# Kernel optimization log

Measured on AMD Instinct MI355X. Metric: run time of the kernel, lower is better.

The kernel has to match this reference:

```python
import jax, jax.numpy as jnp
import numpy as np

NX = 48
N_TILES = 6
C_IN = 16
H = 32            # node_hidden_channels
EH = 64           # edge_hidden_channels
N_STEPS = 4       # num_step_message_passing
N_NODES = N_TILES * NX * NX


def _build_edges(nx, n_tiles):
    # 4-neighbor (up/down/left/right, wraparound) connectivity per tile
    ii = np.arange(nx * nx, dtype=np.int32).reshape(nx, nx)
    srcs, dsts = [], []
    for t in range(n_tiles):
        off = t * nx * nx
        for ax, sh in ((0, 1), (0, -1), (1, 1), (1, -1)):
            srcs.append(off + np.roll(ii, sh, axis=ax).ravel())
            dsts.append(off + ii.ravel())
    return np.concatenate(srcs), np.concatenate(dsts)


def setup_inputs() -> dict:
    key = jax.random.key(0)
    ks = jax.random.split(key, 16)
    src_np, dst_np = _build_edges(NX, N_TILES)
    E = src_np.shape[0]  # 55296
    s = 0.1
    return {
        "in_node_feats": jax.random.normal(ks[0], (2, N_TILES, NX, NX, C_IN), jnp.float32),
        "edge_feats": jax.random.normal(ks[1], (E, 2), jnp.float32),
        "src": jnp.asarray(src_np, jnp.int32),
        "dst": jnp.asarray(dst_np, jnp.int32),
        # project_node_feats: Linear(C_IN,H) -> relu -> Linear(H,H)
        "pW1": jax.random.normal(ks[2], (C_IN, H), jnp.float32) * s,
        "pb1": jnp.zeros((H,), jnp.float32),
        "pW2": jax.random.normal(ks[3], (H, H), jnp.float32) * s,
        "pb2": jnp.zeros((H,), jnp.float32),
        # edge network: Linear(2,EH) -> relu -> Linear(EH, H*H)
        "eW1": jax.random.normal(ks[4], (2, EH), jnp.float32) * s,
        "eb1": jnp.zeros((EH,), jnp.float32),
        "eW2": jax.random.normal(ks[5], (EH, H * H), jnp.float32) * (s / 4.0),
        "eb2": jnp.zeros((H * H,), jnp.float32),
        # NNConv bias
        "conv_b": jnp.zeros((H,), jnp.float32),
        # GRU (single layer): gate order r, z, n (PyTorch)
        "gWih": jax.random.normal(ks[6], (3 * H, H), jnp.float32) * s,
        "gWhh": jax.random.normal(ks[7], (3 * H, H), jnp.float32) * s,
        "gbih": jnp.zeros((3 * H,), jnp.float32),
        "gbhh": jnp.zeros((3 * H,), jnp.float32),
    }


def reference(in_node_feats, edge_feats, src, dst,
              pW1, pb1, pW2, pb2, eW1, eb1, eW2, eb2,
              conv_b, gWih, gWhh, gbih, gbhh):
    shp = in_node_feats.shape           # (B, T, nx, ny, Cin)
    B = shp[0]
    N = shp[1] * shp[2] * shp[3]
    x = in_node_feats.reshape(B, N, shp[-1])
    # project node features
    x = jnp.maximum(x @ pW1 + pb1, 0.0) @ pW2 + pb2      # (B, N, H)
    # per-edge weight matrices (shared across batch and steps)
    We = jnp.maximum(edge_feats @ eW1 + eb1, 0.0) @ eW2 + eb2
    We = We.reshape(-1, H, H)                             # (E, H, H)
    h = x
    seg = jax.vmap(lambda m: jax.ops.segment_sum(m, dst, num_segments=N))
    for _ in range(N_STEPS):
        # NNConv: gather src feats, per-edge matmul, scatter-sum to dst, + bias
        msg = jnp.einsum('beh,eho->beo', x[:, src], We)   # (B, E, H)
        x = jnp.maximum(seg(msg) + conv_b, 0.0)           # relu(conv)
        # GRU cell (seq_len = 1)
        gx = x @ gWih.T + gbih
        gh = h @ gWhh.T + gbhh
        xr, xz, xn = jnp.split(gx, 3, axis=-1)
        hr, hz, hn = jnp.split(gh, 3, axis=-1)
        r = jax.nn.sigmoid(xr + hr)
        z = jax.nn.sigmoid(xz + hz)
        n = jnp.tanh(xn + r * hn)
        h = (1.0 - z) * n + z * h
        x = h
    return x.reshape(shp[:4] + (H,))
```

## Files before the change

kernel.cpp:

```cpp
#include <hip/hip_runtime.h>
#include <stdint.h>

constexpr int NB   = 2;
constexpr int NN   = 13824;
constexpr int NE   = 55296;
constexpr int H    = 32;
constexpr int EHID = 64;
constexpr int HH   = 1024;
constexpr int TILE = 2304;
constexpr int NXC  = 48;

typedef float f32x4 __attribute__((ext_vector_type(4)));
typedef short s16x8 __attribute__((ext_vector_type(8)));
typedef unsigned int u32x2 __attribute__((ext_vector_type(2)));
typedef unsigned int u32x4 __attribute__((ext_vector_type(4)));
typedef __attribute__((address_space(1))) unsigned int as1_uint;
typedef __attribute__((address_space(3))) unsigned int as3_uint;

static __device__ __forceinline__ unsigned short f2bf(float f) {
    unsigned u = __float_as_uint(f);
    return (unsigned short)((u + 0x7fffu + ((u >> 16) & 1u)) >> 16);
}
static __device__ __forceinline__ unsigned packbf(float lo, float hi) {
    return (unsigned)f2bf(lo) | ((unsigned)f2bf(hi) << 16);
}
static __device__ __forceinline__ void gload16(const void* g, void* l) {
    __builtin_amdgcn_global_load_lds((const as1_uint*)g, (as3_uint*)l, 16, 0, 0);
}
static __device__ __forceinline__ float sigf(float v) {
    return 1.0f / (1.0f + __expf(-v));
}
static __device__ __forceinline__ float tanhfast(float v) {
    return 1.0f - 2.0f / (1.0f + __expf(2.0f * v));
}

__global__ void __launch_bounds__(256)
k_pre(const float* __restrict__ ef, const float* __restrict__ eW1,
      const float* __restrict__ eb1, unsigned short* __restrict__ aB,
      const float* __restrict__ eW2, const float* __restrict__ eb2,
      unsigned short* __restrict__ BpT, float* __restrict__ eb2p,
      const float* __restrict__ in, const float* __restrict__ pW1,
      const float* __restrict__ pb1, const float* __restrict__ pW2,
      const float* __restrict__ pb2, float* __restrict__ S0,
      unsigned short* __restrict__ xb0,
      const float* __restrict__ gWih, const float* __restrict__ gWhh,
      unsigned short* __restrict__ gWb) {
    int blk = blockIdx.x;
    if (blk < 3456) {
        int t = blk * 256 + threadIdx.x;
        int e = t >> 4, kq = (t & 15) * 4;
        float f0 = ef[e * 2], f1 = ef[e * 2 + 1];
        u32x2 w;
#pragma unroll
        for (int q = 0; q < 2; q++) {
            int k = kq + q * 2;
            float v0 = fmaxf(f0 * eW1[k]     + f1 * eW1[64 + k]     + eb1[k],     0.f);
            float v1 = fmaxf(f0 * eW1[k + 1] + f1 * eW1[64 + k + 1] + eb1[k + 1], 0.f);
            w[q] = packbf(v0, v1);
        }
        *(u32x2*)(aB + e * 64 + kq) = w;
    } else if (blk < 3520) {
        int t = (blk - 3456) * 256 + threadIdx.x;
        int jp = t >> 4, kq = (t & 15) * 4;
        int src_col = (jp & 31) * 32 + (jp >> 5);
        u32x2 w;
#pragma unroll
        for (int q = 0; q < 2; q++) {
            int k = kq + q * 2;
            w[q] = packbf(eW2[k * HH + src_col], eW2[(k + 1) * HH + src_col]);
        }
        *(u32x2*)(BpT + jp * 64 + kq) = w;
        if (kq == 0) eb2p[jp] = eb2[src_col];
    } else if (blk < 6976) {
        int t = (blk - 3520) * 256 + threadIdx.x;
        int p = t >> 5;
        int l = t & 31;
        float iv = (l < 16) ? in[p * 16 + l] : 0.f;
        float hid = pb1[l];
#pragma unroll
        for (int c = 0; c < 16; c++) hid = fmaf(__shfl(iv, c, 32), pW1[c * H + l], hid);
        hid = fmaxf(hid, 0.f);
        float out = pb2[l];
#pragma unroll
        for (int h = 0; h < 32; h++) out = fmaf(__shfl(hid, h, 32), pW2[h * H + l], out);
        S0[p * H + l]  = out;
        xb0[p * H + l] = f2bf(out);
    } else {
        int idx = (blk - 6976) * 256 + threadIdx.x;
        gWb[idx] = f2bf(idx < 3072 ? gWih[idx] : gWhh[idx - 3072]);
    }
}

__global__ void __launch_bounds__(256)
k_gemm(const unsigned short* __restrict__ Bp, const unsigned short* __restrict__ Ae,
       const float* __restrict__ eb2p, unsigned short* __restrict__ C) {
    __shared__ unsigned char lds[32768] __attribute__((aligned(16)));
    const int tid  = threadIdx.x;
    const int wv   = tid >> 6;
    const int lane = tid & 63;
    const int lr   = lane & 15;
    const int lg   = lane >> 4;
    const int jbt  = blockIdx.x;
    const int ebt  = blockIdx.y;

    const unsigned char* Ag = (const unsigned char*)Bp + (size_t)jbt * 16384;
    const unsigned char* Bg = (const unsigned char*)Ae + (size_t)ebt * 16384;

#pragma unroll
    for (int c = 0; c < 4; c++) {
        int fbase = (wv * 4 + c) * 1024;
        int f  = fbase + lane * 16;
        int sw = f ^ (((f >> 7) & 7) << 4);
        gload16(Ag + sw, lds + fbase);
        gload16(Bg + sw, lds + 16384 + fbase);
    }
    asm volatile("s_waitcnt vmcnt(0)" ::: "memory");
    __syncthreads();

    const int wm = wv >> 1, wn = wv & 1;
    f32x4 acc[4][4] = {};
#pragma unroll
    for (int kk = 0; kk < 2; kk++) {
        s16x8 af[4], bf[4];
#pragma unroll
        for (int i = 0; i < 4; i++) {
            int la = ((wm * 64 + i * 16 + lr) * 64 + kk * 32 + lg * 8) * 2;
            la ^= ((la >> 7) & 7) << 4;
            af[i] = *(const s16x8*)(lds + la);
            int lb = ((wn * 64 + i * 16 + lr) * 64 + kk * 32 + lg * 8) * 2;
            lb ^= ((lb >> 7) & 7) << 4;
            bf[i] = *(const s16x8*)(lds + 16384 + lb);
        }
#pragma unroll
        for (int i = 0; i < 4; i++)
#pragma unroll
            for (int j = 0; j < 4; j++)
                acc[i][j] = __builtin_amdgcn_mfma_f32_16x16x32_bf16(af[i], bf[j], acc[i][j], 0, 0, 0);
    }

    float bias[4][4];
#pragma unroll
    for (int i = 0; i < 4; i++)
#pragma unroll
        for (int r = 0; r < 4; r++)
            bias[i][r] = eb2p[jbt * 128 + wm * 64 + i * 16 + lg * 4 + r];

    __syncthreads();
#pragma unroll
    for (int i = 0; i < 4; i++) {
#pragma unroll
        for (int j = 0; j < 4; j++) {
            int el    = wn * 64 + j * 16 + lr;
            int jbase = wm * 64 + i * 16 + lg * 4;
            int L0 = el * 256 + jbase * 2;
            int ph = L0 ^ ((el & 7) << 4);
            u32x2 w;
            w[0] = packbf(acc[i][j][0] + bias[i][0], acc[i][j][1] + bias[i][1]);
            w[1] = packbf(acc[i][j][2] + bias[i][2], acc[i][j][3] + bias[i][3]);
            *(u32x2*)(lds + ph) = w;
        }
    }
    __syncthreads();

    const int q  = (ebt * 128) / TILE;
    const int i0 = (ebt * 128) % TILE;
    const int tt = q >> 2, kk2 = q & 3;
    const size_t nbase = (size_t)tt * TILE + i0;
#pragma unroll
    for (int pass = 0; pass < 8; pass++) {
        int L2 = pass * 4096 + tid * 16;
        int el = L2 >> 8;
        int ph = L2 ^ ((el & 7) << 4);
        u32x4 v = *(const u32x4*)(lds + ph);
        size_t drow = (nbase + el) * 4 + kk2;
        *(u32x4*)((unsigned char*)C + drow * 2048 + (size_t)jbt * 256 + (L2 & 255)) = v;
    }
}

__global__ void __launch_bounds__(256)
k_step3(const unsigned short* __restrict__ xb_in,
        const float* __restrict__ h_in,
        const unsigned short* __restrict__ WeTn,
        const float* __restrict__ conv_b,
        const unsigned short* __restrict__ gWb,
        const float* __restrict__ gbih, const float* __restrict__ gbhh,
        float* __restrict__ h_out, unsigned short* __restrict__ xb_out) {
    __shared__ unsigned short cv[2][8][32];
    const int tid  = threadIdx.x;
    const int wv   = tid >> 6;
    const int l    = tid & 63;
    const int cl   = l & 15;
    const int kg   = l >> 4;
    const int bsel = cl & 1;
    const int n0   = blockIdx.x * 8;

    int srcs[2][4];
#pragma unroll
    for (int un = 0; un < 2; ++un) {
        int n = n0 + wv * 2 + un;
        int t = n / TILE;
        int i = n - t * TILE;
        int r = i / NXC;
        int c = i - r * NXC;
        int bt = t * TILE;
        int rm = (r == 0) ? NXC - 1 : r - 1;
        int rp = (r == NXC - 1) ? 0 : r + 1;
        int cm = (c == 0) ? NXC - 1 : c - 1;
        int cp = (c == NXC - 1) ? 0 : c + 1;
        srcs[un][0] = bt + rm * NXC + c;
        srcs[un][1] = bt + rp * NXC + c;
        srcs[un][2] = bt + r * NXC + cm;
        srcs[un][3] = bt + r * NXC + cp;
    }

    s16x8 af[2][4][2];
#pragma unroll
    for (int un = 0; un < 2; ++un) {
        const unsigned short* wp = WeTn + ((size_t)(n0 + wv * 2 + un) * 4) * HH;
#pragma unroll
        for (int k = 0; k < 4; ++k) {
            af[un][k][0] = *(const s16x8*)(wp + k * HH + cl * 32 + kg * 8);
            af[un][k][1] = *(const s16x8*)(wp + k * HH + 512 + cl * 32 + kg * 8);
        }
    }

    f32x4 a[2][2] = {};
#pragma unroll
    for (int un = 0; un < 2; ++un) {
#pragma unroll
        for (int k = 0; k < 4; ++k) {
            s16x8 bfr = *(const s16x8*)(xb_in + ((size_t)(bsel * NN + srcs[un][k])) * 32 + kg * 8);
            a[un][0] = __builtin_amdgcn_mfma_f32_16x16x32_bf16(af[un][k][0], bfr, a[un][0], 0, 0, 0);
            a[un][1] = __builtin_amdgcn_mfma_f32_16x16x32_bf16(af[un][k][1], bfr, a[un][1], 0, 0, 0);
        }
    }

    f32x4 cb0 = *(const f32x4*)(conv_b + kg * 4);
    f32x4 cb1 = *(const f32x4*)(conv_b + 16 + kg * 4);
    if (cl < 2) {
#pragma unroll
        for (int un = 0; un < 2; ++un) {
            int nl = wv * 2 + un;
            unsigned* cp32 = (unsigned*)&cv[cl][nl][0];
            cp32[kg * 2]     = packbf(fmaxf(a[un][0][0] + cb0[0], 0.f), fmaxf(a[un][0][1] + cb0[1], 0.f));
            cp32[kg * 2 + 1] = packbf(fmaxf(a[un][0][2] + cb0[2], 0.f), fmaxf(a[un][0][3] + cb0[3], 0.f));
            cp32[8 + kg * 2]     = packbf(fmaxf(a[un][1][0] + cb1[0], 0.f), fmaxf(a[un][1][1] + cb1[1], 0.f));
            cp32[8 + kg * 2 + 1] = packbf(fmaxf(a[un][1][2] + cb1[2], 0.f), fmaxf(a[un][1][3] + cb1[3], 0.f));
        }
    }
    __syncthreads();

    if (wv == 0) {
        s16x8 ax = *(const s16x8*)&cv[cl >> 3][cl & 7][kg * 8];
        s16x8 ah = *(const s16x8*)(xb_in + ((size_t)(cl >> 3) * NN + n0 + (cl & 7)) * 32 + kg * 8);

        f32x4 accx[6], acch[6];
#pragma unroll
        for (int jb = 0; jb < 6; ++jb) {
            s16x8 wx = *(const s16x8*)(gWb + (jb * 16 + cl) * 32 + kg * 8);
            s16x8 wh = *(const s16x8*)(gWb + 3072 + (jb * 16 + cl) * 32 + kg * 8);
            f32x4 z0 = {};
            f32x4 z1 = {};
            accx[jb] = __builtin_amdgcn_mfma_f32_16x16x32_bf16(ax, wx, z0, 0, 0, 0);
            acch[jb] = __builtin_amdgcn_mfma_f32_16x16x32_bf16(ah, wh, z1, 0, 0, 0);
        }

        float bihR[2] = {gbih[cl],      gbih[16 + cl]};
        float bihZ[2] = {gbih[32 + cl], gbih[48 + cl]};
        float bihN[2] = {gbih[64 + cl], gbih[80 + cl]};
        float bhhR[2] = {gbhh[cl],      gbhh[16 + cl]};
        float bhhZ[2] = {gbhh[32 + cl], gbhh[48 + cl]};
        float bhhN[2] = {gbhh[64 + cl], gbhh[80 + cl]};

#pragma unroll
        for (int hb = 0; hb < 2; ++hb) {
#pragma unroll
            for (int ri = 0; ri < 4; ++ri) {
                int rrow = kg * 4 + ri;
                size_t m = (size_t)(rrow >> 3) * NN + n0 + (rrow & 7);
                float rg = sigf(accx[hb][ri] + acch[hb][ri] + bihR[hb] + bhhR[hb]);
                float zg = sigf(accx[2 + hb][ri] + acch[2 + hb][ri] + bihZ[hb] + bhhZ[hb]);
                float ng = tanhfast((accx[4 + hb][ri] + bihN[hb]) +
                                    rg * (acch[4 + hb][ri] + bhhN[hb]));
                float ho = h_in[m * 32 + hb * 16 + cl];
                float hn = fmaf(zg, ho - ng, ng);
                h_out[m * 32 + hb * 16 + cl]  = hn;
                xb_out[m * 32 + hb * 16 + cl] = f2bf(hn);
            }
        }
    }
}

extern "C" void kernel_launch(void* const* d_in, const int* in_sizes, int n_in,
                              void* d_out, int out_size, void* d_ws, size_t ws_size,
                              hipStream_t stream) {
    const float* in_nodes = (const float*)d_in[0];
    const float* ef       = (const float*)d_in[1];
    const float* pW1      = (const float*)d_in[4];
    const float* pb1      = (const float*)d_in[5];
    const float* pW2      = (const float*)d_in[6];
    const float* pb2      = (const float*)d_in[7];
    const float* eW1      = (const float*)d_in[8];
    const float* eb1      = (const float*)d_in[9];
    const float* eW2      = (const float*)d_in[10];
    const float* eb2      = (const float*)d_in[11];
    const float* convb    = (const float*)d_in[12];
    const float* gWih     = (const float*)d_in[13];
    const float* gWhh     = (const float*)d_in[14];
    const float* gbih     = (const float*)d_in[15];
    const float* gbhh     = (const float*)d_in[16];

    unsigned char* ws = (unsigned char*)d_ws;
    unsigned short* WeTn = (unsigned short*)(ws + 0ull);
    unsigned short* aB   = (unsigned short*)(ws + 113246208ull);
    unsigned short* BpT  = (unsigned short*)(ws + 120324096ull);
    float*          eb2p = (float*)         (ws + 120455168ull);
    float*          S0   = (float*)         (ws + 120459264ull);
    float*          S1   = (float*)         (ws + 123998208ull);
    unsigned short* xb0  = (unsigned short*)(ws + 127537152ull);
    unsigned short* xb1  = (unsigned short*)(ws + 129306624ull);
    unsigned short* gWb  = (unsigned short*)(ws + 131076096ull);

    k_pre<<<7000, 256, 0, stream>>>(ef, eW1, eb1, aB, eW2, eb2, BpT, eb2p,
                                    in_nodes, pW1, pb1, pW2, pb2, S0, xb0,
                                    gWih, gWhh, gWb);
    dim3 g3(8, 432);
    k_gemm<<<g3, 256, 0, stream>>>(BpT, aB, eb2p, WeTn);

    float* out = (float*)d_out;
    k_step3<<<1728, 256, 0, stream>>>(xb0, S0, WeTn, convb, gWb, gbih, gbhh, S1, xb1);
    k_step3<<<1728, 256, 0, stream>>>(xb1, S1, WeTn, convb, gWb, gbih, gbhh, S0, xb0);
    k_step3<<<1728, 256, 0, stream>>>(xb0, S0, WeTn, convb, gWb, gbih, gbhh, S1, xb1);
    k_step3<<<1728, 256, 0, stream>>>(xb1, S1, WeTn, convb, gWb, gbih, gbhh, out, xb0);
}
```

Baseline: 217.7 us.

## Fuse edge-weight GEMM into message-passing step, recompute per-edge weights in LDS

Drops the separate kernel that materialized the full per-edge weight tensor (about 113 MB of bf16) in global memory. Each step kernel now recomputes its 64 edges' weight matrices from the edge hidden activations and the second-layer weights with MFMA, stages them in 64 KB of LDS, and feeds them to the message MFMAs. Block size rises from 8 to 16 nodes, so two wavefronts run the GRU stage. This trades a large global write plus four reads of that tensor for recomputing the edge GEMM four times. The larger LDS footprint also lowers occupancy.

```diff
diff --git a/kernel.cpp b/kernel.cpp
--- a/kernel.cpp
+++ b/kernel.cpp
@@ -13,8 +13,6 @@
 typedef float f32x4 __attribute__((ext_vector_type(4)));
 typedef short s16x8 __attribute__((ext_vector_type(8)));
 typedef unsigned int u32x2 __attribute__((ext_vector_type(2)));
-typedef unsigned int u32x4 __attribute__((ext_vector_type(4)));
-typedef __attribute__((address_space(1))) unsigned int as1_uint;
 typedef __attribute__((address_space(3))) unsigned int as3_uint;
 
 static __device__ __forceinline__ unsigned short f2bf(float f) {
@@ -24,8 +22,10 @@
 static __device__ __forceinline__ unsigned packbf(float lo, float hi) {
     return (unsigned)f2bf(lo) | ((unsigned)f2bf(hi) << 16);
 }
-static __device__ __forceinline__ void gload16(const void* g, void* l) {
-    __builtin_amdgcn_global_load_lds((const as1_uint*)g, (as3_uint*)l, 16, 0, 0);
+static __device__ __forceinline__ unsigned cvtpk(float lo, float hi) {
+    unsigned r;
+    asm("v_cvt_pk_bf16_f32 %0, %1, %2" : "=v"(r) : "v"(lo), "v"(hi));
+    return r;
 }
 static __device__ __forceinline__ float sigf(float v) {
     return 1.0f / (1.0f + __expf(-v));
@@ -92,146 +92,97 @@
 }
 
 __global__ void __launch_bounds__(256)
-k_gemm(const unsigned short* __restrict__ Bp, const unsigned short* __restrict__ Ae,
-       const float* __restrict__ eb2p, unsigned short* __restrict__ C) {
-    __shared__ unsigned char lds[32768] __attribute__((aligned(16)));
-    const int tid  = threadIdx.x;
-    const int wv   = tid >> 6;
-    const int lane = tid & 63;
-    const int lr   = lane & 15;
-    const int lg   = lane >> 4;
-    const int jbt  = blockIdx.x;
-    const int ebt  = blockIdx.y;
-
-    const unsigned char* Ag = (const unsigned char*)Bp + (size_t)jbt * 16384;
-    const unsigned char* Bg = (const unsigned char*)Ae + (size_t)ebt * 16384;
-
-#pragma unroll
-    for (int c = 0; c < 4; c++) {
-        int fbase = (wv * 4 + c) * 1024;
-        int f  = fbase + lane * 16;
-        int sw = f ^ (((f >> 7) & 7) << 4);
-        gload16(Ag + sw, lds + fbase);
-        gload16(Bg + sw, lds + 16384 + fbase);
-    }
-    asm volatile("s_waitcnt vmcnt(0)" ::: "memory");
-    __syncthreads();
-
-    const int wm = wv >> 1, wn = wv & 1;
-    f32x4 acc[4][4] = {};
-#pragma unroll
-    for (int kk = 0; kk < 2; kk++) {
-        s16x8 af[4], bf[4];
-#pragma unroll
-        for (int i = 0; i < 4; i++) {
-            int la = ((wm * 64 + i * 16 + lr) * 64 + kk * 32 + lg * 8) * 2;
-            la ^= ((la >> 7) & 7) << 4;
-            af[i] = *(const s16x8*)(lds + la);
-            int lb = ((wn * 64 + i * 16 + lr) * 64 + kk * 32 + lg * 8) * 2;
-            lb ^= ((lb >> 7) & 7) << 4;
-            bf[i] = *(const s16x8*)(lds + 16384 + lb);
-        }
-#pragma unroll
-        for (int i = 0; i < 4; i++)
-#pragma unroll
-            for (int j = 0; j < 4; j++)
-                acc[i][j] = __builtin_amdgcn_mfma_f32_16x16x32_bf16(af[i], bf[j], acc[i][j], 0, 0, 0);
-    }
-
-    float bias[4][4];
-#pragma unroll
-    for (int i = 0; i < 4; i++)
-#pragma unroll
-        for (int r = 0; r < 4; r++)
-            bias[i][r] = eb2p[jbt * 128 + wm * 64 + i * 16 + lg * 4 + r];
-
-    __syncthreads();
-#pragma unroll
-    for (int i = 0; i < 4; i++) {
-#pragma unroll
-        for (int j = 0; j < 4; j++) {
-            int el    = wn * 64 + j * 16 + lr;
-            int jbase = wm * 64 + i * 16 + lg * 4;
-            int L0 = el * 256 + jbase * 2;
-            int ph = L0 ^ ((el & 7) << 4);
-            u32x2 w;
-            w[0] = packbf(acc[i][j][0] + bias[i][0], acc[i][j][1] + bias[i][1]);
-            w[1] = packbf(acc[i][j][2] + bias[i][2], acc[i][j][3] + bias[i][3]);
-            *(u32x2*)(lds + ph) = w;
-        }
-    }
-    __syncthreads();
-
-    const int q  = (ebt * 128) / TILE;
-    const int i0 = (ebt * 128) % TILE;
-    const int tt = q >> 2, kk2 = q & 3;
-    const size_t nbase = (size_t)tt * TILE + i0;
-#pragma unroll
-    for (int pass = 0; pass < 8; pass++) {
-        int L2 = pass * 4096 + tid * 16;
-        int el = L2 >> 8;
-        int ph = L2 ^ ((el & 7) << 4);
-        u32x4 v = *(const u32x4*)(lds + ph);
-        size_t drow = (nbase + el) * 4 + kk2;
-        *(u32x4*)((unsigned char*)C + drow * 2048 + (size_t)jbt * 256 + (L2 & 255)) = v;
-    }
-}
-
-__global__ void __launch_bounds__(256)
-k_step3(const unsigned short* __restrict__ xb_in,
+k_fstep(const unsigned short* __restrict__ xb_in,
         const float* __restrict__ h_in,
-        const unsigned short* __restrict__ WeTn,
+        const unsigned short* __restrict__ aB,
+        const unsigned short* __restrict__ Bp,
+        const float* __restrict__ eb2p,
         const float* __restrict__ conv_b,
         const unsigned short* __restrict__ gWb,
         const float* __restrict__ gbih, const float* __restrict__ gbhh,
         float* __restrict__ h_out, unsigned short* __restrict__ xb_out) {
-    __shared__ unsigned short cv[2][8][32];
+    __shared__ unsigned char smem[65536 + 2048] __attribute__((aligned(16)));
+    unsigned short* cvp = (unsigned short*)(smem + 65536);
+
     const int tid  = threadIdx.x;
     const int wv   = tid >> 6;
     const int l    = tid & 63;
     const int cl   = l & 15;
     const int kg   = l >> 4;
     const int bsel = cl & 1;
-    const int n0   = blockIdx.x * 8;
-
-    int srcs[2][4];
-#pragma unroll
-    for (int un = 0; un < 2; ++un) {
-        int n = n0 + wv * 2 + un;
-        int t = n / TILE;
-        int i = n - t * TILE;
+    const int n0   = blockIdx.x * 16;
+    const int tt   = n0 / TILE;
+    const int i0   = n0 - tt * TILE;
+
+    int srcs[4][4];
+#pragma unroll
+    for (int u = 0; u < 4; ++u) {
+        int n = n0 + wv * 4 + u;
+        int i = n - tt * TILE;
         int r = i / NXC;
         int c = i - r * NXC;
-        int bt = t * TILE;
+        int bt = tt * TILE;
         int rm = (r == 0) ? NXC - 1 : r - 1;
         int rp = (r == NXC - 1) ? 0 : r + 1;
         int cm = (c == 0) ? NXC - 1 : c - 1;
         int cp = (c == NXC - 1) ? 0 : c + 1;
-        srcs[un][0] = bt + rm * NXC + c;
-        srcs[un][1] = bt + rp * NXC + c;
-        srcs[un][2] = bt + r * NXC + cm;
-        srcs[un][3] = bt + r * NXC + cp;
-    }
-
-    s16x8 af[2][4][2];
-#pragma unroll
-    for (int un = 0; un < 2; ++un) {
-        const unsigned short* wp = WeTn + ((size_t)(n0 + wv * 2 + un) * 4) * HH;
-#pragma unroll
-        for (int k = 0; k < 4; ++k) {
-            af[un][k][0] = *(const s16x8*)(wp + k * HH + cl * 32 + kg * 8);
-            af[un][k][1] = *(const s16x8*)(wp + k * HH + 512 + cl * 32 + kg * 8);
-        }
-    }
-
-    f32x4 a[2][2] = {};
-#pragma unroll
-    for (int un = 0; un < 2; ++un) {
-#pragma unroll
-        for (int k = 0; k < 4; ++k) {
-            s16x8 bfr = *(const s16x8*)(xb_in + ((size_t)(bsel * NN + srcs[un][k])) * 32 + kg * 8);
-            a[un][0] = __builtin_amdgcn_mfma_f32_16x16x32_bf16(af[un][k][0], bfr, a[un][0], 0, 0, 0);
-            a[un][1] = __builtin_amdgcn_mfma_f32_16x16x32_bf16(af[un][k][1], bfr, a[un][1], 0, 0, 0);
+        srcs[u][0] = bt + rm * NXC + c;
+        srcs[u][1] = bt + rp * NXC + c;
+        srcs[u][2] = bt + r * NXC + cm;
+        srcs[u][3] = bt + r * NXC + cp;
+    }
+
+    s16x8 bfrag[4][2];
+#pragma unroll
+    for (int d = 0; d < 4; ++d) {
+        const unsigned short* ap = aB + ((size_t)((tt * 4 + d) * TILE + i0 + cl)) * 64;
+#pragma unroll
+        for (int kk = 0; kk < 2; ++kk)
+            bfrag[d][kk] = *(const s16x8*)(ap + kk * 32 + kg * 8);
+    }
+
+    f32x4 a[4][2] = {};
+
+#pragma unroll
+    for (int half = 0; half < 2; ++half) {
+        if (half == 1) __syncthreads();
+
+#pragma unroll
+        for (int it = 0; it < 8; ++it) {
+            int jb = (wv * 8 + it) * 16;
+            int jrow = half * 512 + jb + cl;
+            s16x8 af0 = *(const s16x8*)(Bp + jrow * 64 + kg * 8);
+            s16x8 af1 = *(const s16x8*)(Bp + jrow * 64 + 32 + kg * 8);
+            f32x4 b4  = *(const f32x4*)(eb2p + half * 512 + jb + kg * 4);
+            f32x4 acc[4] = {};
+#pragma unroll
+            for (int d = 0; d < 4; ++d) {
+                acc[d] = __builtin_amdgcn_mfma_f32_16x16x32_bf16(af0, bfrag[d][0], acc[d], 0, 0, 0);
+                acc[d] = __builtin_amdgcn_mfma_f32_16x16x32_bf16(af1, bfrag[d][1], acc[d], 0, 0, 0);
+            }
+#pragma unroll
+            for (int d = 0; d < 4; ++d) {
+                int el = d * 16 + cl;
+                int L  = el * 1024 + (jb + kg * 4) * 2;
+                int ph = L ^ ((el & 7) << 4);
+                u32x2 w;
+                w[0] = cvtpk(acc[d][0] + b4[0], acc[d][1] + b4[1]);
+                w[1] = cvtpk(acc[d][2] + b4[2], acc[d][3] + b4[3]);
+                *(u32x2*)(smem + ph) = w;
+            }
+        }
+        __syncthreads();
+
+#pragma unroll
+        for (int d = 0; d < 4; ++d) {
+#pragma unroll
+            for (int u = 0; u < 4; ++u) {
+                int rl = d * 16 + (wv * 4 + u);
+                int ph = (rl * 1024 + cl * 64 + kg * 16) ^ ((rl & 7) << 4);
+                s16x8 af  = *(const s16x8*)(smem + ph);
+                s16x8 bfr = *(const s16x8*)(xb_in + ((size_t)(bsel * NN + srcs[u][d])) * 32 + kg * 8);
+                a[u][half] = __builtin_amdgcn_mfma_f32_16x16x32_bf16(af, bfr, a[u][half], 0, 0, 0);
+            }
         }
     }
 
@@ -239,20 +190,20 @@
     f32x4 cb1 = *(const f32x4*)(conv_b + 16 + kg * 4);
     if (cl < 2) {
 #pragma unroll
-        for (int un = 0; un < 2; ++un) {
-            int nl = wv * 2 + un;
-            unsigned* cp32 = (unsigned*)&cv[cl][nl][0];
-            cp32[kg * 2]     = packbf(fmaxf(a[un][0][0] + cb0[0], 0.f), fmaxf(a[un][0][1] + cb0[1], 0.f));
-            cp32[kg * 2 + 1] = packbf(fmaxf(a[un][0][2] + cb0[2], 0.f), fmaxf(a[un][0][3] + cb0[3], 0.f));
-            cp32[8 + kg * 2]     = packbf(fmaxf(a[un][1][0] + cb1[0], 0.f), fmaxf(a[un][1][1] + cb1[1], 0.f));
-            cp32[8 + kg * 2 + 1] = packbf(fmaxf(a[un][1][2] + cb1[2], 0.f), fmaxf(a[un][1][3] + cb1[3], 0.f));
+        for (int u = 0; u < 4; ++u) {
+            int nl = wv * 4 + u;
+            unsigned* cp32 = (unsigned*)&cvp[(cl * 16 + nl) * 32];
+            cp32[kg * 2]     = cvtpk(fmaxf(a[u][0][0] + cb0[0], 0.f), fmaxf(a[u][0][1] + cb0[1], 0.f));
+            cp32[kg * 2 + 1] = cvtpk(fmaxf(a[u][0][2] + cb0[2], 0.f), fmaxf(a[u][0][3] + cb0[3], 0.f));
+            cp32[8 + kg * 2]     = cvtpk(fmaxf(a[u][1][0] + cb1[0], 0.f), fmaxf(a[u][1][1] + cb1[1], 0.f));
+            cp32[8 + kg * 2 + 1] = cvtpk(fmaxf(a[u][1][2] + cb1[2], 0.f), fmaxf(a[u][1][3] + cb1[3], 0.f));
         }
     }
     __syncthreads();
 
-    if (wv == 0) {
-        s16x8 ax = *(const s16x8*)&cv[cl >> 3][cl & 7][kg * 8];
-        s16x8 ah = *(const s16x8*)(xb_in + ((size_t)(cl >> 3) * NN + n0 + (cl & 7)) * 32 + kg * 8);
+    if (wv < 2) {
+        s16x8 ax = *(const s16x8*)(cvp + (wv * 16 + cl) * 32 + kg * 8);
+        s16x8 ah = *(const s16x8*)(xb_in + ((size_t)wv * NN + n0 + cl) * 32 + kg * 8);
 
         f32x4 accx[6], acch[6];
 #pragma unroll
@@ -277,7 +228,7 @@
 #pragma unroll
             for (int ri = 0; ri < 4; ++ri) {
                 int rrow = kg * 4 + ri;
-                size_t m = (size_t)(rrow >> 3) * NN + n0 + (rrow & 7);
+                size_t m = (size_t)wv * NN + n0 + rrow;
                 float rg = sigf(accx[hb][ri] + acch[hb][ri] + bihR[hb] + bhhR[hb]);
                 float zg = sigf(accx[2 + hb][ri] + acch[2 + hb][ri] + bihZ[hb] + bhhZ[hb]);
                 float ng = tanhfast((accx[4 + hb][ri] + bihN[hb]) +
@@ -311,25 +262,26 @@
     const float* gbhh     = (const float*)d_in[16];
 
     unsigned char* ws = (unsigned char*)d_ws;
-    unsigned short* WeTn = (unsigned short*)(ws + 0ull);
-    unsigned short* aB   = (unsigned short*)(ws + 113246208ull);
-    unsigned short* BpT  = (unsigned short*)(ws + 120324096ull);
-    float*          eb2p = (float*)         (ws + 120455168ull);
-    float*          S0   = (float*)         (ws + 120459264ull);
-    float*          S1   = (float*)         (ws + 123998208ull);
-    unsigned short* xb0  = (unsigned short*)(ws + 127537152ull);
-    unsigned short* xb1  = (unsigned short*)(ws + 129306624ull);
-    unsigned short* gWb  = (unsigned short*)(ws + 131076096ull);
+    unsigned short* aB   = (unsigned short*)(ws + 0ull);
+    unsigned short* BpT  = (unsigned short*)(ws + 7077888ull);
+    float*          eb2p = (float*)         (ws + 7208960ull);
+    float*          S0   = (float*)         (ws + 7213056ull);
+    float*          S1   = (float*)         (ws + 10752000ull);
+    unsigned short* xb0  = (unsigned short*)(ws + 14290944ull);
+    unsigned short* xb1  = (unsigned short*)(ws + 16060416ull);
+    unsigned short* gWb  = (unsigned short*)(ws + 17829888ull);
 
     k_pre<<<7000, 256, 0, stream>>>(ef, eW1, eb1, aB, eW2, eb2, BpT, eb2p,
                                     in_nodes, pW1, pb1, pW2, pb2, S0, xb0,
                                     gWih, gWhh, gWb);
-    dim3 g3(8, 432);
-    k_gemm<<<g3, 256, 0, stream>>>(BpT, aB, eb2p, WeTn);
 
     float* out = (float*)d_out;
-    k_step3<<<1728, 256, 0, stream>>>(xb0, S0, WeTn, convb, gWb, gbih, gbhh, S1, xb1);
-    k_step3<<<1728, 256, 0, stream>>>(xb1, S1, WeTn, convb, gWb, gbih, gbhh, S0, xb0);
-    k_step3<<<1728, 256, 0, stream>>>(xb0, S0, WeTn, convb, gWb, gbih, gbhh, S1, xb1);
-    k_step3<<<1728, 256, 0, stream>>>(xb1, S1, WeTn, convb, gWb, gbih, gbhh, out, xb0);
-}
+    k_fstep<<<NN / 16, 256, 0, stream>>>(xb0, S0, aB, BpT, eb2p, convb, gWb,
+                                         gbih, gbhh, S1, xb1);
+    k_fstep<<<NN / 16, 256, 0, stream>>>(xb1, S1, aB, BpT, eb2p, convb, gWb,
+                                         gbih, gbhh, S0, xb0);
+    k_fstep<<<NN / 16, 256, 0, stream>>>(xb0, S0, aB, BpT, eb2p, convb, gWb,
+                                         gbih, gbhh, S1, xb1);
+    k_fstep<<<NN / 16, 256, 0, stream>>>(xb1, S1, aB, BpT, eb2p, convb, gWb,
+                                         gbih, gbhh, out, xb0);
+}
```

Measured after the change: 255.4 us. 17.3% more time.

## Fuse four message-passing steps into one cooperative kernel with grid sync

Applied to the files above, without the earlier changes.

Replaces the four separate step launches with one cooperative kernel that runs all steps and separates them with grid-wide syncs, falling back to per-step launches if the cooperative launch fails. Each block now handles 16 nodes instead of 8, with 4 nodes per wave, and two waves do the GRU so both batch entries are covered. Source-index computation is done once and reused across steps. This aims to cut launch gaps and raise per-block work, but grid.sync has its own cost and occupancy limits how many blocks can be co-resident.

```diff
diff --git a/kernel.cpp b/kernel.cpp
--- a/kernel.cpp
+++ b/kernel.cpp
@@ -1,5 +1,8 @@
 #include <hip/hip_runtime.h>
+#include <hip/hip_cooperative_groups.h>
 #include <stdint.h>
+
+namespace cg = cooperative_groups;
 
 constexpr int NB   = 2;
 constexpr int NN   = 13824;
@@ -14,7 +17,6 @@
 typedef short s16x8 __attribute__((ext_vector_type(8)));
 typedef unsigned int u32x2 __attribute__((ext_vector_type(2)));
 typedef unsigned int u32x4 __attribute__((ext_vector_type(4)));
-typedef __attribute__((address_space(1))) unsigned int as1_uint;
 typedef __attribute__((address_space(3))) unsigned int as3_uint;
 
 static __device__ __forceinline__ unsigned short f2bf(float f) {
@@ -23,9 +25,6 @@
 }
 static __device__ __forceinline__ unsigned packbf(float lo, float hi) {
     return (unsigned)f2bf(lo) | ((unsigned)f2bf(hi) << 16);
-}
-static __device__ __forceinline__ void gload16(const void* g, void* l) {
-    __builtin_amdgcn_global_load_lds((const as1_uint*)g, (as3_uint*)l, 16, 0, 0);
 }
 static __device__ __forceinline__ float sigf(float v) {
     return 1.0f / (1.0f + __expf(-v));
@@ -111,8 +110,12 @@
         int fbase = (wv * 4 + c) * 1024;
         int f  = fbase + lane * 16;
         int sw = f ^ (((f >> 7) & 7) << 4);
-        gload16(Ag + sw, lds + fbase);
-        gload16(Bg + sw, lds + 16384 + fbase);
+        __builtin_amdgcn_global_load_lds(
+            (const __attribute__((address_space(1))) unsigned int*)(Ag + sw),
+            (as3_uint*)(lds + fbase), 16, 0, 0);
+        __builtin_amdgcn_global_load_lds(
+            (const __attribute__((address_space(1))) unsigned int*)(Bg + sw),
+            (as3_uint*)(lds + 16384 + fbase), 16, 0, 0);
     }
     asm volatile("s_waitcnt vmcnt(0)" ::: "memory");
     __syncthreads();
@@ -177,61 +180,30 @@
     }
 }
 
-__global__ void __launch_bounds__(256)
-k_step3(const unsigned short* __restrict__ xb_in,
-        const float* __restrict__ h_in,
-        const unsigned short* __restrict__ WeTn,
-        const float* __restrict__ conv_b,
-        const unsigned short* __restrict__ gWb,
-        const float* __restrict__ gbih, const float* __restrict__ gbhh,
-        float* __restrict__ h_out, unsigned short* __restrict__ xb_out) {
-    __shared__ unsigned short cv[2][8][32];
-    const int tid  = threadIdx.x;
-    const int wv   = tid >> 6;
-    const int l    = tid & 63;
-    const int cl   = l & 15;
-    const int kg   = l >> 4;
-    const int bsel = cl & 1;
-    const int n0   = blockIdx.x * 8;
-
-    int srcs[2][4];
-#pragma unroll
-    for (int un = 0; un < 2; ++un) {
-        int n = n0 + wv * 2 + un;
-        int t = n / TILE;
-        int i = n - t * TILE;
-        int r = i / NXC;
-        int c = i - r * NXC;
-        int bt = t * TILE;
-        int rm = (r == 0) ? NXC - 1 : r - 1;
-        int rp = (r == NXC - 1) ? 0 : r + 1;
-        int cm = (c == 0) ? NXC - 1 : c - 1;
-        int cp = (c == NXC - 1) ? 0 : c + 1;
-        srcs[un][0] = bt + rm * NXC + c;
-        srcs[un][1] = bt + rp * NXC + c;
-        srcs[un][2] = bt + r * NXC + cm;
-        srcs[un][3] = bt + r * NXC + cp;
-    }
-
-    s16x8 af[2][4][2];
-#pragma unroll
-    for (int un = 0; un < 2; ++un) {
-        const unsigned short* wp = WeTn + ((size_t)(n0 + wv * 2 + un) * 4) * HH;
-#pragma unroll
-        for (int k = 0; k < 4; ++k) {
-            af[un][k][0] = *(const s16x8*)(wp + k * HH + cl * 32 + kg * 8);
-            af[un][k][1] = *(const s16x8*)(wp + k * HH + 512 + cl * 32 + kg * 8);
-        }
-    }
-
-    f32x4 a[2][2] = {};
-#pragma unroll
-    for (int un = 0; un < 2; ++un) {
-#pragma unroll
-        for (int k = 0; k < 4; ++k) {
-            s16x8 bfr = *(const s16x8*)(xb_in + ((size_t)(bsel * NN + srcs[un][k])) * 32 + kg * 8);
-            a[un][0] = __builtin_amdgcn_mfma_f32_16x16x32_bf16(af[un][k][0], bfr, a[un][0], 0, 0, 0);
-            a[un][1] = __builtin_amdgcn_mfma_f32_16x16x32_bf16(af[un][k][1], bfr, a[un][1], 0, 0, 0);
+static __device__ __forceinline__ void step_body(
+    const unsigned short* __restrict__ xb_in, const float* __restrict__ h_in,
+    float* __restrict__ h_out, unsigned short* __restrict__ xb_out,
+    const unsigned short* __restrict__ WeTn, const float* __restrict__ conv_b,
+    const unsigned short* __restrict__ gWb,
+    const float* __restrict__ gbih, const float* __restrict__ gbhh,
+    unsigned short* cvp, int wv, int cl, int kg, int bsel, int n0,
+    const int srcs[4][4]) {
+
+    f32x4 a[4][2] = {};
+#pragma unroll
+    for (int u = 0; u < 4; ++u) {
+        const unsigned short* wp = WeTn + ((size_t)(n0 + wv * 4 + u) * 4) * HH;
+        s16x8 af[4][2];
+#pragma unroll
+        for (int d = 0; d < 4; ++d) {
+            af[d][0] = *(const s16x8*)(wp + d * HH + cl * 32 + kg * 8);
+            af[d][1] = *(const s16x8*)(wp + d * HH + 512 + cl * 32 + kg * 8);
+        }
+#pragma unroll
+        for (int d = 0; d < 4; ++d) {
+            s16x8 bfr = *(const s16x8*)(xb_in + ((size_t)(bsel * NN + srcs[u][d])) * 32 + kg * 8);
+            a[u][0] = __builtin_amdgcn_mfma_f32_16x16x32_bf16(af[d][0], bfr, a[u][0], 0, 0, 0);
+            a[u][1] = __builtin_amdgcn_mfma_f32_16x16x32_bf16(af[d][1], bfr, a[u][1], 0, 0, 0);
         }
     }
 
@@ -239,20 +211,22 @@
     f32x4 cb1 = *(const f32x4*)(conv_b + 16 + kg * 4);
     if (cl < 2) {
 #pragma unroll
-        for (int un = 0; un < 2; ++un) {
-            int nl = wv * 2 + un;
-            unsigned* cp32 = (unsigned*)&cv[cl][nl][0];
-            cp32[kg * 2]     = packbf(fmaxf(a[un][0][0] + cb0[0], 0.f), fmaxf(a[un][0][1] + cb0[1], 0.f));
-            cp32[kg * 2 + 1] = packbf(fmaxf(a[un][0][2] + cb0[2], 0.f), fmaxf(a[un][0][3] + cb0[3], 0.f));
-            cp32[8 + kg * 2]     = packbf(fmaxf(a[un][1][0] + cb1[0], 0.f), fmaxf(a[un][1][1] + cb1[1], 0.f));
-            cp32[8 + kg * 2 + 1] = packbf(fmaxf(a[un][1][2] + cb1[2], 0.f), fmaxf(a[un][1][3] + cb1[3], 0.f));
+        for (int u = 0; u < 4; ++u) {
+            int nl = wv * 4 + u;
+            unsigned* cp32 = (unsigned*)(cvp + (cl * 16 + nl) * 32);
+            cp32[kg * 2]     = packbf(fmaxf(a[u][0][0] + cb0[0], 0.f), fmaxf(a[u][0][1] + cb0[1], 0.f));
+            cp32[kg * 2 + 1] = packbf(fmaxf(a[u][0][2] + cb0[2], 0.f), fmaxf(a[u][0][3] + cb0[3], 0.f));
+            cp32[8 + kg * 2]     = packbf(fmaxf(a[u][1][0] + cb1[0], 0.f), fmaxf(a[u][1][1] + cb1[1], 0.f));
+            cp32[8 + kg * 2 + 1] = packbf(fmaxf(a[u][1][2] + cb1[2], 0.f), fmaxf(a[u][1][3] + cb1[3], 0.f));
         }
     }
     __syncthreads();
 
-    if (wv == 0) {
-        s16x8 ax = *(const s16x8*)&cv[cl >> 3][cl & 7][kg * 8];
-        s16x8 ah = *(const s16x8*)(xb_in + ((size_t)(cl >> 3) * NN + n0 + (cl & 7)) * 32 + kg * 8);
+    if (wv < 2) {
+        const size_t mbase = (size_t)wv * NN + n0;
+
+        s16x8 ax = *(const s16x8*)(cvp + (wv * 16 + cl) * 32 + kg * 8);
+        s16x8 ah = *(const s16x8*)(xb_in + (mbase + cl) * 32 + kg * 8);
 
         f32x4 accx[6], acch[6];
 #pragma unroll
@@ -274,21 +248,96 @@
 
 #pragma unroll
         for (int hb = 0; hb < 2; ++hb) {
+            const float* hp = h_in  + mbase * 32 + kg * 128 + hb * 16 + cl;
+            float*       op = h_out + mbase * 32 + kg * 128 + hb * 16 + cl;
+            unsigned short* xp = xb_out + mbase * 32 + kg * 128 + hb * 16 + cl;
 #pragma unroll
             for (int ri = 0; ri < 4; ++ri) {
-                int rrow = kg * 4 + ri;
-                size_t m = (size_t)(rrow >> 3) * NN + n0 + (rrow & 7);
                 float rg = sigf(accx[hb][ri] + acch[hb][ri] + bihR[hb] + bhhR[hb]);
                 float zg = sigf(accx[2 + hb][ri] + acch[2 + hb][ri] + bihZ[hb] + bhhZ[hb]);
                 float ng = tanhfast((accx[4 + hb][ri] + bihN[hb]) +
                                     rg * (acch[4 + hb][ri] + bhhN[hb]));
-                float ho = h_in[m * 32 + hb * 16 + cl];
+                float ho = hp[ri * 32];
                 float hn = fmaf(zg, ho - ng, ng);
-                h_out[m * 32 + hb * 16 + cl]  = hn;
-                xb_out[m * 32 + hb * 16 + cl] = f2bf(hn);
+                op[ri * 32] = hn;
+                xp[ri * 32] = f2bf(hn);
             }
         }
     }
+}
+
+static __device__ __forceinline__ void calc_srcs(int n0, int wv, int srcs[4][4]) {
+    const int tt = n0 / TILE;
+#pragma unroll
+    for (int u = 0; u < 4; ++u) {
+        int n = n0 + wv * 4 + u;
+        int i = n - tt * TILE;
+        int r = i / NXC;
+        int c = i - r * NXC;
+        int bt = tt * TILE;
+        int rm = (r == 0) ? NXC - 1 : r - 1;
+        int rp = (r == NXC - 1) ? 0 : r + 1;
+        int cm = (c == 0) ? NXC - 1 : c - 1;
+        int cp = (c == NXC - 1) ? 0 : c + 1;
+        srcs[u][0] = bt + rm * NXC + c;
+        srcs[u][1] = bt + rp * NXC + c;
+        srcs[u][2] = bt + r * NXC + cm;
+        srcs[u][3] = bt + r * NXC + cp;
+    }
+}
+
+__global__ void __launch_bounds__(256, 4)
+k_steps(unsigned short* xb0, unsigned short* xb1,
+        float* S0, float* S1, float* out,
+        const unsigned short* __restrict__ WeTn, const float* __restrict__ conv_b,
+        const unsigned short* __restrict__ gWb,
+        const float* __restrict__ gbih, const float* __restrict__ gbhh) {
+    cg::grid_group grid = cg::this_grid();
+    __shared__ unsigned short cv[2 * 16 * 32];
+
+    const int tid  = threadIdx.x;
+    const int wv   = tid >> 6;
+    const int l    = tid & 63;
+    const int cl   = l & 15;
+    const int kg   = l >> 4;
+    const int bsel = cl & 1;
+    const int n0   = blockIdx.x * 16;
+
+    int srcs[4][4];
+    calc_srcs(n0, wv, srcs);
+
+    step_body(xb0, S0, S1, xb1, WeTn, conv_b, gWb, gbih, gbhh,
+              cv, wv, cl, kg, bsel, n0, srcs);
+    grid.sync();
+    step_body(xb1, S1, S0, xb0, WeTn, conv_b, gWb, gbih, gbhh,
+              cv, wv, cl, kg, bsel, n0, srcs);
+    grid.sync();
+    step_body(xb0, S0, S1, xb1, WeTn, conv_b, gWb, gbih, gbhh,
+              cv, wv, cl, kg, bsel, n0, srcs);
+    grid.sync();
+    step_body(xb1, S1, out, xb0, WeTn, conv_b, gWb, gbih, gbhh,
+              cv, wv, cl, kg, bsel, n0, srcs);
+}
+
+__global__ void __launch_bounds__(256, 4)
+k_step1(const unsigned short* __restrict__ xb_in, const float* __restrict__ h_in,
+        float* __restrict__ h_out, unsigned short* __restrict__ xb_out,
+        const unsigned short* __restrict__ WeTn, const float* __restrict__ conv_b,
+        const unsigned short* __restrict__ gWb,
+        const float* __restrict__ gbih, const float* __restrict__ gbhh) {
+    __shared__ unsigned short cv[2 * 16 * 32];
+    const int tid  = threadIdx.x;
+    const int wv   = tid >> 6;
+    const int l    = tid & 63;
+    const int cl   = l & 15;
+    const int kg   = l >> 4;
+    const int bsel = cl & 1;
+    const int n0   = blockIdx.x * 16;
+
+    int srcs[4][4];
+    calc_srcs(n0, wv, srcs);
+    step_body(xb_in, h_in, h_out, xb_out, WeTn, conv_b, gWb, gbih, gbhh,
+              cv, wv, cl, kg, bsel, n0, srcs);
 }
 
 extern "C" void kernel_launch(void* const* d_in, const int* in_sizes, int n_in,
@@ -328,8 +377,13 @@
     k_gemm<<<g3, 256, 0, stream>>>(BpT, aB, eb2p, WeTn);
 
     float* out = (float*)d_out;
-    k_step3<<<1728, 256, 0, stream>>>(xb0, S0, WeTn, convb, gWb, gbih, gbhh, S1, xb1);
-    k_step3<<<1728, 256, 0, stream>>>(xb1, S1, WeTn, convb, gWb, gbih, gbhh, S0, xb0);
-    k_step3<<<1728, 256, 0, stream>>>(xb0, S0, WeTn, convb, gWb, gbih, gbhh, S1, xb1);
-    k_step3<<<1728, 256, 0, stream>>>(xb1, S1, WeTn, convb, gWb, gbih, gbhh, out, xb0);
-}
+    void* args[] = {&xb0, &xb1, &S0, &S1, &out, &WeTn, &convb, &gWb, &gbih, &gbhh};
+    hipError_t err = hipLaunchCooperativeKernel((void*)k_steps, dim3(864), dim3(256),
+                                                args, 0, stream);
+    if (err != hipSuccess) {
+        k_step1<<<NN / 16, 256, 0, stream>>>(xb0, S0, S1, xb1, WeTn, convb, gWb, gbih, gbhh);
+        k_step1<<<NN / 16, 256, 0, stream>>>(xb1, S1, S0, xb0, WeTn, convb, gWb, gbih, gbhh);
+        k_step1<<<NN / 16, 256, 0, stream>>>(xb0, S0, S1, xb1, WeTn, convb, gWb, gbih, gbhh);
+        k_step1<<<NN / 16, 256, 0, stream>>>(xb1, S1, out, xb0, WeTn, convb, gWb, gbih, gbhh);
+    }
+}
```

Result: slower. 565.6 us (+159.8%).

## Stage per-node edge weights in LDS via async global-to-LDS loads with swizzle

Applied to the files above, without the earlier changes.

The GEMM epilogue now writes the per-edge weight matrices with an XOR swizzle. The step kernel streams each block's 64KB of edge weights into LDS using global_load_lds and reads them back through the matching swizzled addresses. Before, each lane loaded weight fragments straight from global memory. The goal is fully coalesced, asynchronous bulk loads that overlap with the neighbor gathers, plus bank-conflict-free LDS reads. The cost is 65KB of LDS per block, which caps occupancy to about two blocks per CU and adds a block-wide barrier before the MFMAs.

```diff
diff --git a/kernel.cpp b/kernel.cpp
--- a/kernel.cpp
+++ b/kernel.cpp
@@ -23,9 +23,6 @@
 }
 static __device__ __forceinline__ unsigned packbf(float lo, float hi) {
     return (unsigned)f2bf(lo) | ((unsigned)f2bf(hi) << 16);
-}
-static __device__ __forceinline__ void gload16(const void* g, void* l) {
-    __builtin_amdgcn_global_load_lds((const as1_uint*)g, (as3_uint*)l, 16, 0, 0);
 }
 static __device__ __forceinline__ float sigf(float v) {
     return 1.0f / (1.0f + __expf(-v));
@@ -111,8 +108,10 @@
         int fbase = (wv * 4 + c) * 1024;
         int f  = fbase + lane * 16;
         int sw = f ^ (((f >> 7) & 7) << 4);
-        gload16(Ag + sw, lds + fbase);
-        gload16(Bg + sw, lds + 16384 + fbase);
+        __builtin_amdgcn_global_load_lds((const as1_uint*)(Ag + sw),
+                                         (as3_uint*)(lds + fbase), 16, 0, 0);
+        __builtin_amdgcn_global_load_lds((const as1_uint*)(Bg + sw),
+                                         (as3_uint*)(lds + 16384 + fbase), 16, 0, 0);
     }
     asm volatile("s_waitcnt vmcnt(0)" ::: "memory");
     __syncthreads();
@@ -164,7 +163,7 @@
 
     const int q  = (ebt * 128) / TILE;
     const int i0 = (ebt * 128) % TILE;
-    const int tt = q >> 2, kk2 = q & 3;
+    const int tt = q >> 2, dd = q & 3;
     const size_t nbase = (size_t)tt * TILE + i0;
 #pragma unroll
     for (int pass = 0; pass < 8; pass++) {
@@ -172,20 +171,24 @@
         int el = L2 >> 8;
         int ph = L2 ^ ((el & 7) << 4);
         u32x4 v = *(const u32x4*)(lds + ph);
-        size_t drow = (nbase + el) * 4 + kk2;
-        *(u32x4*)((unsigned char*)C + drow * 2048 + (size_t)jbt * 256 + (L2 & 255)) = v;
+        size_t drow = (nbase + el) * 4 + dd;
+        int jg = jbt * 128 + ((L2 & 255) >> 1);
+        int lb = (jg * 2) ^ (((jg >> 5) & 7) << 4);
+        *(u32x4*)((unsigned char*)C + drow * 2048 + lb) = v;
     }
 }
 
 __global__ void __launch_bounds__(256)
-k_step3(const unsigned short* __restrict__ xb_in,
+k_stepB(const unsigned short* __restrict__ xb_in,
         const float* __restrict__ h_in,
-        const unsigned short* __restrict__ WeTn,
+        const unsigned char* __restrict__ WeTnS,
         const float* __restrict__ conv_b,
         const unsigned short* __restrict__ gWb,
         const float* __restrict__ gbih, const float* __restrict__ gbhh,
         float* __restrict__ h_out, unsigned short* __restrict__ xb_out) {
-    __shared__ unsigned short cv[2][8][32];
+    __shared__ unsigned char stage[65536 + 1024] __attribute__((aligned(16)));
+    unsigned short* cvp = (unsigned short*)(stage + 65536);
+
     const int tid  = threadIdx.x;
     const int wv   = tid >> 6;
     const int l    = tid & 63;
@@ -193,45 +196,55 @@
     const int kg   = l >> 4;
     const int bsel = cl & 1;
     const int n0   = blockIdx.x * 8;
+    const int tt   = n0 / TILE;
+
+    const unsigned char* gsrc = WeTnS + (size_t)n0 * 8192;
+#pragma unroll
+    for (int i = 0; i < 16; i++) {
+        int off = wv * 16384 + i * 1024 + (l << 4);
+        __builtin_amdgcn_global_load_lds((const as1_uint*)(gsrc + off),
+                                         (as3_uint*)(stage + off), 16, 0, 0);
+    }
 
     int srcs[2][4];
 #pragma unroll
-    for (int un = 0; un < 2; ++un) {
-        int n = n0 + wv * 2 + un;
-        int t = n / TILE;
-        int i = n - t * TILE;
+    for (int u = 0; u < 2; ++u) {
+        int n = n0 + wv * 2 + u;
+        int i = n - tt * TILE;
         int r = i / NXC;
         int c = i - r * NXC;
-        int bt = t * TILE;
+        int bt = tt * TILE;
         int rm = (r == 0) ? NXC - 1 : r - 1;
         int rp = (r == NXC - 1) ? 0 : r + 1;
         int cm = (c == 0) ? NXC - 1 : c - 1;
         int cp = (c == NXC - 1) ? 0 : c + 1;
-        srcs[un][0] = bt + rm * NXC + c;
-        srcs[un][1] = bt + rp * NXC + c;
-        srcs[un][2] = bt + r * NXC + cm;
-        srcs[un][3] = bt + r * NXC + cp;
-    }
-
-    s16x8 af[2][4][2];
-#pragma unroll
-    for (int un = 0; un < 2; ++un) {
-        const unsigned short* wp = WeTn + ((size_t)(n0 + wv * 2 + un) * 4) * HH;
-#pragma unroll
-        for (int k = 0; k < 4; ++k) {
-            af[un][k][0] = *(const s16x8*)(wp + k * HH + cl * 32 + kg * 8);
-            af[un][k][1] = *(const s16x8*)(wp + k * HH + 512 + cl * 32 + kg * 8);
-        }
-    }
-
+        srcs[u][0] = bt + rm * NXC + c;
+        srcs[u][1] = bt + rp * NXC + c;
+        srcs[u][2] = bt + r * NXC + cm;
+        srcs[u][3] = bt + r * NXC + cp;
+    }
+    s16x8 bfr[2][4];
+#pragma unroll
+    for (int u = 0; u < 2; ++u)
+#pragma unroll
+        for (int d = 0; d < 4; ++d)
+            bfr[u][d] = *(const s16x8*)(xb_in + ((size_t)(bsel * NN + srcs[u][d])) * 32 + kg * 8);
+
+    asm volatile("s_waitcnt vmcnt(0)" ::: "memory");
+    __syncthreads();
+
+    const int lb0 = (cl * 64 + kg * 16) ^ ((cl & 7) << 4);
+    const int lb1 = (1024 + cl * 64 + kg * 16) ^ ((cl & 7) << 4);
     f32x4 a[2][2] = {};
 #pragma unroll
-    for (int un = 0; un < 2; ++un) {
-#pragma unroll
-        for (int k = 0; k < 4; ++k) {
-            s16x8 bfr = *(const s16x8*)(xb_in + ((size_t)(bsel * NN + srcs[un][k])) * 32 + kg * 8);
-            a[un][0] = __builtin_amdgcn_mfma_f32_16x16x32_bf16(af[un][k][0], bfr, a[un][0], 0, 0, 0);
-            a[un][1] = __builtin_amdgcn_mfma_f32_16x16x32_bf16(af[un][k][1], bfr, a[un][1], 0, 0, 0);
+    for (int u = 0; u < 2; ++u) {
+        const unsigned char* np = stage + (wv * 2 + u) * 8192;
+#pragma unroll
+        for (int d = 0; d < 4; ++d) {
+            s16x8 af0 = *(const s16x8*)(np + d * 2048 + lb0);
+            s16x8 af1 = *(const s16x8*)(np + d * 2048 + lb1);
+            a[u][0] = __builtin_amdgcn_mfma_f32_16x16x32_bf16(af0, bfr[u][d], a[u][0], 0, 0, 0);
+            a[u][1] = __builtin_amdgcn_mfma_f32_16x16x32_bf16(af1, bfr[u][d], a[u][1], 0, 0, 0);
         }
     }
 
@@ -239,19 +252,19 @@
     f32x4 cb1 = *(const f32x4*)(conv_b + 16 + kg * 4);
     if (cl < 2) {
 #pragma unroll
-        for (int un = 0; un < 2; ++un) {
-            int nl = wv * 2 + un;
-            unsigned* cp32 = (unsigned*)&cv[cl][nl][0];
-            cp32[kg * 2]     = packbf(fmaxf(a[un][0][0] + cb0[0], 0.f), fmaxf(a[un][0][1] + cb0[1], 0.f));
-            cp32[kg * 2 + 1] = packbf(fmaxf(a[un][0][2] + cb0[2], 0.f), fmaxf(a[un][0][3] + cb0[3], 0.f));
-            cp32[8 + kg * 2]     = packbf(fmaxf(a[un][1][0] + cb1[0], 0.f), fmaxf(a[un][1][1] + cb1[1], 0.f));
-            cp32[8 + kg * 2 + 1] = packbf(fmaxf(a[un][1][2] + cb1[2], 0.f), fmaxf(a[un][1][3] + cb1[3], 0.f));
+        for (int u = 0; u < 2; ++u) {
+            int nl = wv * 2 + u;
+            unsigned* cp32 = (unsigned*)(cvp + (cl * 8 + nl) * 32);
+            cp32[kg * 2]     = packbf(fmaxf(a[u][0][0] + cb0[0], 0.f), fmaxf(a[u][0][1] + cb0[1], 0.f));
+            cp32[kg * 2 + 1] = packbf(fmaxf(a[u][0][2] + cb0[2], 0.f), fmaxf(a[u][0][3] + cb0[3], 0.f));
+            cp32[8 + kg * 2]     = packbf(fmaxf(a[u][1][0] + cb1[0], 0.f), fmaxf(a[u][1][1] + cb1[1], 0.f));
+            cp32[8 + kg * 2 + 1] = packbf(fmaxf(a[u][1][2] + cb1[2], 0.f), fmaxf(a[u][1][3] + cb1[3], 0.f));
         }
     }
     __syncthreads();
 
     if (wv == 0) {
-        s16x8 ax = *(const s16x8*)&cv[cl >> 3][cl & 7][kg * 8];
+        s16x8 ax = *(const s16x8*)(cvp + ((cl >> 3) * 8 + (cl & 7)) * 32 + kg * 8);
         s16x8 ah = *(const s16x8*)(xb_in + ((size_t)(cl >> 3) * NN + n0 + (cl & 7)) * 32 + kg * 8);
 
         f32x4 accx[6], acch[6];
@@ -311,7 +324,7 @@
     const float* gbhh     = (const float*)d_in[16];
 
     unsigned char* ws = (unsigned char*)d_ws;
-    unsigned short* WeTn = (unsigned short*)(ws + 0ull);
+    unsigned char*  WeTnS = (unsigned char*) (ws + 0ull);
     unsigned short* aB   = (unsigned short*)(ws + 113246208ull);
     unsigned short* BpT  = (unsigned short*)(ws + 120324096ull);
     float*          eb2p = (float*)         (ws + 120455168ull);
@@ -325,11 +338,11 @@
                                     in_nodes, pW1, pb1, pW2, pb2, S0, xb0,
                                     gWih, gWhh, gWb);
     dim3 g3(8, 432);
-    k_gemm<<<g3, 256, 0, stream>>>(BpT, aB, eb2p, WeTn);
+    k_gemm<<<g3, 256, 0, stream>>>(BpT, aB, eb2p, (unsigned short*)WeTnS);
 
     float* out = (float*)d_out;
-    k_step3<<<1728, 256, 0, stream>>>(xb0, S0, WeTn, convb, gWb, gbih, gbhh, S1, xb1);
-    k_step3<<<1728, 256, 0, stream>>>(xb1, S1, WeTn, convb, gWb, gbih, gbhh, S0, xb0);
-    k_step3<<<1728, 256, 0, stream>>>(xb0, S0, WeTn, convb, gWb, gbih, gbhh, S1, xb1);
-    k_step3<<<1728, 256, 0, stream>>>(xb1, S1, WeTn, convb, gWb, gbih, gbhh, out, xb0);
-}
+    k_stepB<<<NN / 8, 256, 0, stream>>>(xb0, S0, WeTnS, convb, gWb, gbih, gbhh, S1, xb1);
+    k_stepB<<<NN / 8, 256, 0, stream>>>(xb1, S1, WeTnS, convb, gWb, gbih, gbhh, S0, xb0);
+    k_stepB<<<NN / 8, 256, 0, stream>>>(xb0, S0, WeTnS, convb, gWb, gbih, gbhh, S1, xb1);
+    k_stepB<<<NN / 8, 256, 0, stream>>>(xb1, S1, WeTnS, convb, gWb, gbih, gbhh, out, xb0);
+}
```

Measured after the change: 231.8 us. 1.06x slower.
